# Kernel tuning notes

Measured on AMD Instinct MI355X. Metric: run time of the kernel, lower is better.

The kernel has to match this reference:

```python
import jax, jax.numpy as jnp
import numpy as np

N, E, D_NLP, D_EMB = 100000, 500000, 768, 128


def setup_inputs() -> dict:
    key = jax.random.key(0)
    ks = jax.random.split(key, 6)
    z = jax.random.normal(ks[0], (N, D_EMB), jnp.float32)
    z0 = jax.random.normal(ks[1], (N, D_NLP), jnp.float32)
    edge_index = jax.random.randint(ks[2], (2, E), 0, N)
    w0 = jax.random.normal(ks[3], (D_EMB, D_NLP), jnp.float32) / np.sqrt(D_NLP)
    prelu_a = jnp.full((1,), 0.25, jnp.float32)  # torch PReLU default init
    w1 = jax.random.normal(ks[4], (1, 3 * D_EMB), jnp.float32) / np.sqrt(3 * D_EMB)
    b1 = jnp.zeros((1,), jnp.float32)
    return {"z": z, "z0": z0, "edge_index": edge_index, "w0": w0,
            "prelu_a": prelu_a, "w1": w1, "b1": b1}


def reference(z, z0, edge_index, w0, prelu_a, w1, b1):
    # qid = elementwise max of the two endpoint rows, shifted to start at 0
    qid = jnp.max(edge_index[0:2], axis=0)
    qid = qid - qid.min()
    # lin0 (no bias) + PReLU with scalar slope
    h = z0[qid] @ w0.T                       # [E, D_EMB]
    x0 = jnp.where(h >= 0, h, prelu_a[0] * h)
    emb1 = z[edge_index[0]]                  # [E, D_EMB]
    emb2 = z[edge_index[1]]                  # [E, D_EMB]
    # lin1(concat([emb1, emb2, x0])) == sum of three matvecs; avoids a [E, 3*D] concat
    w1a, w1b, w1c = w1[0, :D_EMB], w1[0, D_EMB:2 * D_EMB], w1[0, 2 * D_EMB:]
    out = emb1 @ w1a + emb2 @ w1b + x0 @ w1c + b1[0]
    return out  # [E]
```

## Files before the change

kernel.cpp:

```cpp
#include <hip/hip_runtime.h>
#include <hip/hip_bf16.h>
#include <stdint.h>

#define D_EMB 128
#define D_NLP 768
#define BM 64
#define BK 64
#define NKC (D_NLP / BK)

typedef __attribute__((ext_vector_type(8))) short bf16x8;
typedef __attribute__((ext_vector_type(4))) float f32x4;
typedef __attribute__((ext_vector_type(8))) unsigned short u16x8;

__device__ __forceinline__ unsigned short f2bf(float f) {
  unsigned u = __builtin_bit_cast(unsigned, f);
  u += 0x7fffu + ((u >> 16) & 1u);
  return (unsigned short)(u >> 16);
}

__device__ __forceinline__ bf16x8 pack8(const float4& a, const float4& b) {
  u16x8 v;
  v[0] = __builtin_bit_cast(unsigned short, __float2bfloat16(a.x));
  v[1] = __builtin_bit_cast(unsigned short, __float2bfloat16(a.y));
  v[2] = __builtin_bit_cast(unsigned short, __float2bfloat16(a.z));
  v[3] = __builtin_bit_cast(unsigned short, __float2bfloat16(a.w));
  v[4] = __builtin_bit_cast(unsigned short, __float2bfloat16(b.x));
  v[5] = __builtin_bit_cast(unsigned short, __float2bfloat16(b.y));
  v[6] = __builtin_bit_cast(unsigned short, __float2bfloat16(b.z));
  v[7] = __builtin_bit_cast(unsigned short, __float2bfloat16(b.w));
  return __builtin_bit_cast(bf16x8, v);
}

__global__ void kw(const float* __restrict__ w0, unsigned short* __restrict__ w0s,
                   int* __restrict__ mn) {
  if (blockIdx.x == 0 && threadIdx.x == 0) mn[0] = 0x7fffffff;
  int t = blockIdx.x * 256 + threadIdx.x;
  if (t >= (D_EMB * D_NLP) / 8) return;
  int u = t & 7, row = (t >> 3) & 127, kc = t >> 10;
  const float4* src = (const float4*)(w0 + (size_t)row * D_NLP + kc * BK + ((u ^ (row & 7)) * 8));
  float4 v0 = src[0], v1 = src[1];
  u16x8 o;
  o[0] = f2bf(v0.x); o[1] = f2bf(v0.y); o[2] = f2bf(v0.z); o[3] = f2bf(v0.w);
  o[4] = f2bf(v1.x); o[5] = f2bf(v1.y); o[6] = f2bf(v1.z); o[7] = f2bf(v1.w);
  *(u16x8*)(w0s + (size_t)t * 8) = o;
}

__global__ void km(const int* __restrict__ ei, int E, int* __restrict__ mn) {
  int t = blockIdx.x * blockDim.x + threadIdx.x;
  int stride = gridDim.x * blockDim.x;
  int m = 0x7fffffff;
  for (int e = t; e < E; e += stride) {
    int a = ei[e], b = ei[E + e];
    int q = a > b ? a : b;
    m = q < m ? q : m;
  }
  #pragma unroll
  for (int off = 32; off; off >>= 1) {
    int o = __shfl_xor(m, off);
    m = o < m ? o : m;
  }
  if ((threadIdx.x & 63) == 0) atomicMin(mn, m);
}

__global__ __launch_bounds__(256) void kc(
    const float* __restrict__ z0, const float* __restrict__ z,
    const unsigned short* __restrict__ w0s, const float* __restrict__ w1,
    const float* __restrict__ prelu_a, float* __restrict__ sv,
    float* __restrict__ ta, float* __restrict__ tb, int N) {
  __shared__ unsigned short Bb[4][D_EMB * BK];

  const int tid = threadIdx.x;
  const int lane = tid & 63;
  const int wave = tid >> 6;
  const int kg = lane >> 4;
  const int col = lane & 15;
  const int myrow = blockIdx.x * BM + wave * 16 + col;
  const int arow_g = min(myrow, N - 1);
  const float* aBase = z0 + (size_t)arow_g * D_NLP + kg * 8;

  f32x4 acc[8];
  #pragma unroll
  for (int c = 0; c < 8; ++c) acc[c] = (f32x4){0.f, 0.f, 0.f, 0.f};

  float4 fa[4][4];

  auto loadA = [&](int slot, int t) {
    const float4* p0 = (const float4*)(aBase + t * BK);
    const float4* p1 = (const float4*)(aBase + t * BK + 32);
    fa[slot][0] = p0[0]; fa[slot][1] = p0[1];
    fa[slot][2] = p1[0]; fa[slot][3] = p1[1];
  };

  auto stageB = [&](int t, int buf) {
    const unsigned short* g = w0s + (size_t)t * (D_EMB * BK) + (size_t)tid * 8;
    #pragma unroll
    for (int p = 0; p < 4; ++p) {
      __builtin_amdgcn_global_load_lds(
          (const __attribute__((address_space(1))) void*)(g + p * 256 * 8),
          (__attribute__((address_space(3))) void*)&Bb[buf][(wave * 64 + p * 256) * 8],
          16, 0, 0);
    }
  };

  loadA(0, 0); stageB(0, 0);
  loadA(1, 1); stageB(1, 1);
  loadA(2, 2); stageB(2, 2);

  #pragma unroll
  for (int t = 0; t < NKC; ++t) {
    if (t <= NKC - 3)      asm volatile("s_waitcnt vmcnt(16)" ::: "memory");
    else if (t == NKC - 2) asm volatile("s_waitcnt vmcnt(8)" ::: "memory");
    else                   asm volatile("s_waitcnt vmcnt(0)" ::: "memory");
    __builtin_amdgcn_s_barrier();
    if (t + 3 < NKC) {
      loadA((t + 3) & 3, t + 3);
      stageB(t + 3, (t + 3) & 3);
    }
    __builtin_amdgcn_sched_barrier(0);

    const float4* f = fa[t & 3];
    bf16x8 af0 = pack8(f[0], f[1]);
    bf16x8 af1 = pack8(f[2], f[3]);

    const unsigned short* Bbuf = Bb[t & 3];
    #pragma unroll
    for (int ks = 0; ks < 2; ++ks) {
      bf16x8 af = ks == 0 ? af0 : af1;
      #pragma unroll
      for (int c = 0; c < 8; ++c) {
        int brow = c * 16 + col;
        bf16x8 bfr = *(const bf16x8*)&Bbuf[(brow * 8 + ((ks * 4 + kg) ^ (brow & 7))) * 8];
        acc[c] = __builtin_amdgcn_mfma_f32_16x16x32_bf16(af, bfr, acc[c], 0, 0, 0);
      }
    }
  }

  float ap = prelu_a[0];
  float ssum[4] = {0.f, 0.f, 0.f, 0.f};
  #pragma unroll
  for (int c = 0; c < 8; ++c) {
    float wc = w1[2 * D_EMB + c * 16 + col];
    #pragma unroll
    for (int i = 0; i < 4; ++i) {
      float h = acc[c][i];
      float x = h >= 0.f ? h : ap * h;
      ssum[i] += x * wc;
    }
  }
  #pragma unroll
  for (int off = 1; off < 16; off <<= 1) {
    #pragma unroll
    for (int i = 0; i < 4; ++i) ssum[i] += __shfl_xor(ssum[i], off);
  }
  if (col == 0) {
    int rbase = blockIdx.x * BM + wave * 16 + kg * 4;
    #pragma unroll
    for (int i = 0; i < 4; ++i) {
      int r = rbase + i;
      if (r < N) sv[r] = ssum[i];
    }
  }

  {
    const float* zp = z + (size_t)arow_g * D_EMB + kg * 32;
    const float4* wa4 = (const float4*)(w1 + kg * 32);
    const float4* wb4 = (const float4*)(w1 + D_EMB + kg * 32);
    float pa = 0.f, pb = 0.f;
    #pragma unroll
    for (int i = 0; i < 8; ++i) {
      float4 zv = ((const float4*)zp)[i];
      float4 wa = wa4[i];
      float4 wb = wb4[i];
      pa += zv.x * wa.x + zv.y * wa.y + zv.z * wa.z + zv.w * wa.w;
      pb += zv.x * wb.x + zv.y * wb.y + zv.z * wb.z + zv.w * wb.w;
    }
    pa += __shfl_xor(pa, 16); pa += __shfl_xor(pa, 32);
    pb += __shfl_xor(pb, 16); pb += __shfl_xor(pb, 32);
    if (kg == 0 && myrow < N) { ta[myrow] = pa; tb[myrow] = pb; }
  }
}

__global__ void kd(const int* __restrict__ ei, const int* __restrict__ mn,
                   const float* __restrict__ ta, const float* __restrict__ tb,
                   const float* __restrict__ sv, const float* __restrict__ b1,
                   float* __restrict__ out, int E) {
  int e = blockIdx.x * blockDim.x + threadIdx.x;
  if (e >= E) return;
  int i0 = ei[e], i1 = ei[E + e];
  int q = (i0 > i1 ? i0 : i1) - mn[0];
  out[e] = ta[i0] + tb[i1] + sv[q] + b1[0];
}

extern "C" void kernel_launch(void* const* d_in, const int* in_sizes, int n_in,
                              void* d_out, int out_size, void* d_ws, size_t ws_size,
                              hipStream_t stream) {
  const float* z  = (const float*)d_in[0];
  const float* z0 = (const float*)d_in[1];
  const int*   ei = (const int*)d_in[2];
  const float* w0 = (const float*)d_in[3];
  const float* pa = (const float*)d_in[4];
  const float* w1 = (const float*)d_in[5];
  const float* b1 = (const float*)d_in[6];
  float* out = (float*)d_out;
  const int N = in_sizes[0] / D_EMB;
  const int E = in_sizes[2] / 2;

  char* ws = (char*)d_ws;
  int* mn = (int*)ws;
  unsigned short* w0s = (unsigned short*)(ws + 256);
  float* ta = (float*)(ws + 256 + 196608);
  float* tb = ta + N;
  float* sv = tb + N;

  kw<<<(D_EMB * D_NLP / 8 + 255) / 256, 256, 0, stream>>>(w0, w0s, mn);
  km<<<256, 256, 0, stream>>>(ei, E, mn);
  kc<<<(N + BM - 1) / BM, 256, 0, stream>>>(z0, z, w0s, w1, pa, sv, ta, tb, N);
  kd<<<(E + 255) / 256, 256, 0, stream>>>(ei, mn, ta, tb, sv, b1, out, E);
}
```

Before: 130.5 us.

## Restructure GEMM k-loop into six 128-wide super-steps with double buffering

The main GEMM kernel's K loop changes from twelve 64-wide steps with a 4-deep LDS ring to six 128-wide super-steps with two LDS buffers and two register sets of A fragments. Each step issues loads two ahead, after a second barrier that protects buffer reuse. The goal is fewer barriers and waitcnt points per block and more MFMA work between synchronizations. In exchange the prefetch depth is shorter, there is an extra barrier per step, and the A-fragment register footprint grows.

```diff
diff --git a/kernel.cpp b/kernel.cpp
--- a/kernel.cpp
+++ b/kernel.cpp
@@ -5,8 +5,7 @@
 #define D_EMB 128
 #define D_NLP 768
 #define BM 64
-#define BK 64
-#define NKC (D_NLP / BK)
+#define NSC 6
 
 typedef __attribute__((ext_vector_type(8))) short bf16x8;
 typedef __attribute__((ext_vector_type(4))) float f32x4;
@@ -37,7 +36,7 @@
   int t = blockIdx.x * 256 + threadIdx.x;
   if (t >= (D_EMB * D_NLP) / 8) return;
   int u = t & 7, row = (t >> 3) & 127, kc = t >> 10;
-  const float4* src = (const float4*)(w0 + (size_t)row * D_NLP + kc * BK + ((u ^ (row & 7)) * 8));
+  const float4* src = (const float4*)(w0 + (size_t)row * D_NLP + kc * 64 + ((u ^ (row & 7)) * 8));
   float4 v0 = src[0], v1 = src[1];
   u16x8 o;
   o[0] = f2bf(v0.x); o[1] = f2bf(v0.y); o[2] = f2bf(v0.z); o[3] = f2bf(v0.w);
@@ -62,12 +61,62 @@
   if ((threadIdx.x & 63) == 0) atomicMin(mn, m);
 }
 
+#define LOADA2(F, SC) do {                                                   \
+    _Pragma("unroll")                                                        \
+    for (int _s = 0; _s < 4; ++_s) {                                         \
+      const float4* _p = (const float4*)(aBase + (SC) * 128 + _s * 32);      \
+      F[2 * _s] = _p[0];                                                     \
+      F[2 * _s + 1] = _p[1];                                                 \
+    }                                                                        \
+  } while (0)
+
+#define STAGEB(SC, BUF) do {                                                 \
+    const unsigned short* _g = w0s + (size_t)(SC) * 16384 + (size_t)tid * 8; \
+    _Pragma("unroll")                                                        \
+    for (int _p = 0; _p < 8; ++_p) {                                         \
+      __builtin_amdgcn_global_load_lds(                                      \
+          (const __attribute__((address_space(1))) void*)(_g + _p * 2048),   \
+          (__attribute__((address_space(3))) void*)&Bb[BUF][(_p * 256 + wave * 64) * 8], \
+          16, 0, 0);                                                         \
+    }                                                                        \
+  } while (0)
+
+#define SUPER(T, F, VM) do {                                                 \
+    asm volatile("s_waitcnt vmcnt(" #VM ")" ::: "memory");                   \
+    __builtin_amdgcn_s_barrier();                                            \
+    __builtin_amdgcn_sched_barrier(0);                                       \
+    bf16x8 _af0 = pack8(F[0], F[1]);                                         \
+    bf16x8 _af1 = pack8(F[2], F[3]);                                         \
+    bf16x8 _af2 = pack8(F[4], F[5]);                                         \
+    bf16x8 _af3 = pack8(F[6], F[7]);                                         \
+    _Pragma("unroll")                                                        \
+    for (int _s = 0; _s < 4; ++_s) {                                         \
+      bf16x8 _af = _s == 0 ? _af0 : _s == 1 ? _af1 : _s == 2 ? _af2 : _af3;  \
+      const int _h = _s >> 1, _sl = _s & 1;                                  \
+      _Pragma("unroll")                                                      \
+      for (int _c = 0; _c < 8; ++_c) {                                       \
+        int _brow = _c * 16 + col;                                           \
+        bf16x8 _bf = *(const bf16x8*)&Bb[(T) & 1][_h * 8192 +                \
+            (_brow * 8 + (((_sl * 4 + kg)) ^ (_brow & 7))) * 8];             \
+        acc[_c] = __builtin_amdgcn_mfma_f32_16x16x32_bf16(_af, _bf, acc[_c], 0, 0, 0); \
+      }                                                                      \
+    }                                                                        \
+    if ((T) + 2 < NSC) {                                                     \
+      __builtin_amdgcn_sched_barrier(0);                                     \
+      __builtin_amdgcn_s_barrier();    \
+      __builtin_amdgcn_sched_barrier(0);                                     \
+      LOADA2(F, (T) + 2);                                                    \
+      STAGEB((T) + 2, (T) & 1);                                              \
+      __builtin_amdgcn_sched_barrier(0);                                     \
+    }                                                                        \
+  } while (0)
+
 __global__ __launch_bounds__(256) void kc(
     const float* __restrict__ z0, const float* __restrict__ z,
     const unsigned short* __restrict__ w0s, const float* __restrict__ w1,
     const float* __restrict__ prelu_a, float* __restrict__ sv,
     float* __restrict__ ta, float* __restrict__ tb, int N) {
-  __shared__ unsigned short Bb[4][D_EMB * BK];
+  __shared__ unsigned short Bb[2][16384];
 
   const int tid = threadIdx.x;
   const int lane = tid & 63;
@@ -82,58 +131,17 @@
   #pragma unroll
   for (int c = 0; c < 8; ++c) acc[c] = (f32x4){0.f, 0.f, 0.f, 0.f};
 
-  float4 fa[4][4];
-
-  auto loadA = [&](int slot, int t) {
-    const float4* p0 = (const float4*)(aBase + t * BK);
-    const float4* p1 = (const float4*)(aBase + t * BK + 32);
-    fa[slot][0] = p0[0]; fa[slot][1] = p0[1];
-    fa[slot][2] = p1[0]; fa[slot][3] = p1[1];
-  };
-
-  auto stageB = [&](int t, int buf) {
-    const unsigned short* g = w0s + (size_t)t * (D_EMB * BK) + (size_t)tid * 8;
-    #pragma unroll
-    for (int p = 0; p < 4; ++p) {
-      __builtin_amdgcn_global_load_lds(
-          (const __attribute__((address_space(1))) void*)(g + p * 256 * 8),
-          (__attribute__((address_space(3))) void*)&Bb[buf][(wave * 64 + p * 256) * 8],
-          16, 0, 0);
-    }
-  };
-
-  loadA(0, 0); stageB(0, 0);
-  loadA(1, 1); stageB(1, 1);
-  loadA(2, 2); stageB(2, 2);
-
-  #pragma unroll
-  for (int t = 0; t < NKC; ++t) {
-    if (t <= NKC - 3)      asm volatile("s_waitcnt vmcnt(16)" ::: "memory");
-    else if (t == NKC - 2) asm volatile("s_waitcnt vmcnt(8)" ::: "memory");
-    else                   asm volatile("s_waitcnt vmcnt(0)" ::: "memory");
-    __builtin_amdgcn_s_barrier();
-    if (t + 3 < NKC) {
-      loadA((t + 3) & 3, t + 3);
-      stageB(t + 3, (t + 3) & 3);
-    }
-    __builtin_amdgcn_sched_barrier(0);
-
-    const float4* f = fa[t & 3];
-    bf16x8 af0 = pack8(f[0], f[1]);
-    bf16x8 af1 = pack8(f[2], f[3]);
-
-    const unsigned short* Bbuf = Bb[t & 3];
-    #pragma unroll
-    for (int ks = 0; ks < 2; ++ks) {
-      bf16x8 af = ks == 0 ? af0 : af1;
-      #pragma unroll
-      for (int c = 0; c < 8; ++c) {
-        int brow = c * 16 + col;
-        bf16x8 bfr = *(const bf16x8*)&Bbuf[(brow * 8 + ((ks * 4 + kg) ^ (brow & 7))) * 8];
-        acc[c] = __builtin_amdgcn_mfma_f32_16x16x32_bf16(af, bfr, acc[c], 0, 0, 0);
-      }
-    }
-  }
+  float4 fa0[8], fa1[8];
+
+  LOADA2(fa0, 0); STAGEB(0, 0);
+  LOADA2(fa1, 1); STAGEB(1, 1);
+
+  SUPER(0, fa0, 16);
+  SUPER(1, fa1, 16);
+  SUPER(2, fa0, 16);
+  SUPER(3, fa1, 16);
+  SUPER(4, fa0, 16);
+  SUPER(5, fa1, 0);
 
   float ap = prelu_a[0];
   float ssum[4] = {0.f, 0.f, 0.f, 0.f};
```

New measurement: 126.4 us. 1.03x faster.

## Stage z0 tiles through LDS via async loads with triple-buffered A

Applied to the files above, without the earlier changes.

The fp32 A operand (z0 rows) is now fetched with global_load_lds into a swizzled, triple-buffered LDS region instead of register prefetch four stages deep. B staging drops to double buffering, and the wait counts are adjusted to match. This frees many vector registers and moves A loads onto the async LDS path. In exchange it raises LDS use to 80 KB of dynamic shared memory per block, which can cut occupancy, and it adds LDS reads for A.

```diff
diff --git a/kernel.cpp b/kernel.cpp
--- a/kernel.cpp
+++ b/kernel.cpp
@@ -37,7 +37,7 @@
   int t = blockIdx.x * 256 + threadIdx.x;
   if (t >= (D_EMB * D_NLP) / 8) return;
   int u = t & 7, row = (t >> 3) & 127, kc = t >> 10;
-  const float4* src = (const float4*)(w0 + (size_t)row * D_NLP + kc * BK + ((u ^ (row & 7)) * 8));
+  const float4* src = (const float4*)(w0 + (size_t)row * D_NLP + kc * 64 + ((u ^ (row & 7)) * 8));
   float4 v0 = src[0], v1 = src[1];
   u16x8 o;
   o[0] = f2bf(v0.x); o[1] = f2bf(v0.y); o[2] = f2bf(v0.z); o[3] = f2bf(v0.w);
@@ -67,28 +67,38 @@
     const unsigned short* __restrict__ w0s, const float* __restrict__ w1,
     const float* __restrict__ prelu_a, float* __restrict__ sv,
     float* __restrict__ ta, float* __restrict__ tb, int N) {
-  __shared__ unsigned short Bb[4][D_EMB * BK];
+  extern __shared__ char smem[];
+  float* Al = (float*)smem;
+  unsigned short* Bl = (unsigned short*)(smem + 49152);
 
   const int tid = threadIdx.x;
   const int lane = tid & 63;
   const int wave = tid >> 6;
   const int kg = lane >> 4;
   const int col = lane & 15;
-  const int myrow = blockIdx.x * BM + wave * 16 + col;
+  const int s16 = lane & 15;
+  const int hl = lane >> 4;
+  const int r0 = blockIdx.x * BM;
+  const int myrow = r0 + wave * 16 + col;
   const int arow_g = min(myrow, N - 1);
-  const float* aBase = z0 + (size_t)arow_g * D_NLP + kg * 8;
-
-  f32x4 acc[8];
-  #pragma unroll
-  for (int c = 0; c < 8; ++c) acc[c] = (f32x4){0.f, 0.f, 0.f, 0.f};
-
-  float4 fa[4][4];
-
-  auto loadA = [&](int slot, int t) {
-    const float4* p0 = (const float4*)(aBase + t * BK);
-    const float4* p1 = (const float4*)(aBase + t * BK + 32);
-    fa[slot][0] = p0[0]; fa[slot][1] = p0[1];
-    fa[slot][2] = p1[0]; fa[slot][3] = p1[1];
+
+  const float* aSrc[4];
+  #pragma unroll
+  for (int p = 0; p < 4; ++p) {
+    int rl = p * 4 + hl;
+    int rg = min(r0 + wave * 16 + rl, N - 1);
+    int cu = s16 ^ (rl & 7);
+    aSrc[p] = z0 + (size_t)rg * D_NLP + cu * 4;
+  }
+
+  auto stageA = [&](int t, int buf) {
+    #pragma unroll
+    for (int p = 0; p < 4; ++p) {
+      __builtin_amdgcn_global_load_lds(
+          (const __attribute__((address_space(1))) void*)(aSrc[p] + t * BK),
+          (__attribute__((address_space(3))) void*)&Al[buf * 4096 + (wave * 16 + p * 4) * 64],
+          16, 0, 0);
+    }
   };
 
   auto stageB = [&](int t, int buf) {
@@ -97,35 +107,39 @@
     for (int p = 0; p < 4; ++p) {
       __builtin_amdgcn_global_load_lds(
           (const __attribute__((address_space(1))) void*)(g + p * 256 * 8),
-          (__attribute__((address_space(3))) void*)&Bb[buf][(wave * 64 + p * 256) * 8],
+          (__attribute__((address_space(3))) void*)&Bl[buf * 8192 + (wave * 64 + p * 256) * 8],
           16, 0, 0);
     }
   };
 
-  loadA(0, 0); stageB(0, 0);
-  loadA(1, 1); stageB(1, 1);
-  loadA(2, 2); stageB(2, 2);
+  f32x4 acc[8];
+  #pragma unroll
+  for (int c = 0; c < 8; ++c) acc[c] = (f32x4){0.f, 0.f, 0.f, 0.f};
+
+  stageB(0, 0);
+  stageA(0, 0);
+  stageA(1, 1);
+
+  const int arow_l = (wave * 16 + col) * 64;
+  const int asw = col & 7;
 
   #pragma unroll
   for (int t = 0; t < NKC; ++t) {
-    if (t <= NKC - 3)      asm volatile("s_waitcnt vmcnt(16)" ::: "memory");
-    else if (t == NKC - 2) asm volatile("s_waitcnt vmcnt(8)" ::: "memory");
-    else                   asm volatile("s_waitcnt vmcnt(0)" ::: "memory");
+    if (t < NKC - 1) asm volatile("s_waitcnt vmcnt(4)" ::: "memory");
+    else             asm volatile("s_waitcnt vmcnt(0)" ::: "memory");
     __builtin_amdgcn_s_barrier();
-    if (t + 3 < NKC) {
-      loadA((t + 3) & 3, t + 3);
-      stageB(t + 3, (t + 3) & 3);
-    }
+    if (t + 1 < NKC) stageB(t + 1, (t + 1) & 1);
+    if (t + 2 < NKC) stageA(t + 2, (t + 2) % 3);
     __builtin_amdgcn_sched_barrier(0);
 
-    const float4* f = fa[t & 3];
-    bf16x8 af0 = pack8(f[0], f[1]);
-    bf16x8 af1 = pack8(f[2], f[3]);
-
-    const unsigned short* Bbuf = Bb[t & 3];
+    const float* Ab = Al + (t % 3) * 4096;
+    const unsigned short* Bbuf = Bl + (t & 1) * 8192;
     #pragma unroll
     for (int ks = 0; ks < 2; ++ks) {
-      bf16x8 af = ks == 0 ? af0 : af1;
+      int u0 = ks * 8 + kg * 2;
+      float4 lo = *(const float4*)&Ab[arow_l + ((u0)     ^ asw) * 4];
+      float4 hi = *(const float4*)&Ab[arow_l + ((u0 + 1) ^ asw) * 4];
+      bf16x8 af = pack8(lo, hi);
       #pragma unroll
       for (int c = 0; c < 8; ++c) {
         int brow = c * 16 + col;
@@ -153,7 +167,7 @@
     for (int i = 0; i < 4; ++i) ssum[i] += __shfl_xor(ssum[i], off);
   }
   if (col == 0) {
-    int rbase = blockIdx.x * BM + wave * 16 + kg * 4;
+    int rbase = r0 + wave * 16 + kg * 4;
     #pragma unroll
     for (int i = 0; i < 4; ++i) {
       int r = rbase + i;
@@ -212,8 +226,11 @@
   float* tb = ta + N;
   float* sv = tb + N;
 
+  hipFuncSetAttribute((const void*)kc,
+                      hipFuncAttributeMaxDynamicSharedMemorySize, 81920);
+
   kw<<<(D_EMB * D_NLP / 8 + 255) / 256, 256, 0, stream>>>(w0, w0s, mn);
   km<<<256, 256, 0, stream>>>(ei, E, mn);
-  kc<<<(N + BM - 1) / BM, 256, 0, stream>>>(z0, z, w0s, w1, pa, sv, ta, tb, N);
+  kc<<<(N + BM - 1) / BM, 256, 81920, stream>>>(z0, z, w0s, w1, pa, sv, ta, tb, N);
   kd<<<(E + 255) / 256, 256, 0, stream>>>(ei, mn, ta, tb, sv, b1, out, E);
 }
```

New measurement: 120.4 us. 1.08x faster.
